# Kernel optimization log

Measured on AMD Instinct MI355X. Metric: run time of the kernel, lower is better.

Reference implementation:

```python
import jax, jax.numpy as jnp
import numpy as np

R_CUT = 5.0
N_NODES = 50000
N_EDGES = 400000
N_GRAPHS = 2500
D = 128        # embedding_size (hardcoded by torch.split(..., 128))
N_RBF = 20
N_BLOCKS = 3
PI = 3.141592653589793


def setup_inputs() -> dict:
    key = jax.random.key(0)
    ks = jax.random.split(key, 32)
    w = lambda k, s: (jax.random.normal(k, s) * 0.05).astype(jnp.float32)
    z = jax.random.randint(ks[0], (N_NODES,), 0, 100)
    edges = jax.random.randint(ks[1], (N_EDGES, 2), 0, N_NODES)
    r_ij = jax.random.uniform(ks[2], (N_EDGES, 1), minval=0.8, maxval=R_CUT, dtype=jnp.float32)
    d = jax.random.normal(ks[3], (N_EDGES, 3), dtype=jnp.float32)
    r_ij_normalized = d / jnp.linalg.norm(d, axis=1, keepdims=True)
    graph_idx = jax.random.randint(ks[4], (N_NODES,), 0, N_GRAPHS)
    return {
        "z": z, "edges": edges, "r_ij": r_ij,
        "r_ij_normalized": r_ij_normalized, "graph_idx": graph_idx,
        "emb": w(ks[5], (100, D)),
        # message blocks (stacked over N_BLOCKS)
        "msg_w1": w(ks[6], (N_BLOCKS, D, D)),   "msg_b1": w(ks[7], (N_BLOCKS, D)),
        "msg_w2": w(ks[8], (N_BLOCKS, D, 3 * D)), "msg_b2": w(ks[9], (N_BLOCKS, 3 * D)),
        "rbf_w": w(ks[10], (N_BLOCKS, N_RBF, 3 * D)), "rbf_b": w(ks[11], (N_BLOCKS, 3 * D)),
        # update blocks
        "upd_U": w(ks[12], (N_BLOCKS, D, D)), "upd_V": w(ks[13], (N_BLOCKS, D, D)),
        "upd_w1": w(ks[14], (N_BLOCKS, 2 * D, D)), "upd_b1": w(ks[15], (N_BLOCKS, D)),
        "upd_w2": w(ks[16], (N_BLOCKS, D, 3 * D)), "upd_b2": w(ks[17], (N_BLOCKS, 3 * D)),
        # readout
        "blue_w1": w(ks[18], (D, D)), "blue_b1": w(ks[19], (D,)),
        "blue_w2": w(ks[20], (D, 1)), "blue_b2": w(ks[21], (1,)),
    }


def _rbf(r, r_cut):
    n = jnp.arange(1, N_RBF + 1, dtype=r.dtype)  # [20]
    return jnp.sin(n * PI / r_cut * r) / r        # [E,20]


def _fcut(r, r_cut):
    return jnp.where(r <= r_cut, 0.5 * (jnp.cos(PI * r / r_cut) + 1.0), 0.0)


def painn_forward(z, edges, r_ij, r_ij_normalized, graph_idx, emb,
                  msg_w1, msg_b1, msg_w2, msg_b2, rbf_w, rbf_b,
                  upd_U, upd_V, upd_w1, upd_b1, upd_w2, upd_b2,
                  blue_w1, blue_b1, blue_w2, blue_b2):
    silu = jax.nn.silu
    src = edges[:, 1]  # gathered (neighbor j)
    dst = edges[:, 0]  # scattered (center i)
    s = emb[z]                                           # [N,128]
    v = jnp.zeros((s.shape[0], 3, D), dtype=r_ij.dtype)  # [N,3,128]
    rbf = _rbf(r_ij, R_CUT)                              # [E,20]
    f_c = _fcut(r_ij, R_CUT)                             # [E,1]
    for i in range(N_BLOCKS):
        # --- message block ---
        rbf_fcut = (rbf @ rbf_w[i] + rbf_b[i]) * f_c            # [E,384]
        s_pass = silu(s @ msg_w1[i] + msg_b1[i]) @ msg_w2[i] + msg_b2[i]  # [N,384]
        pass_out = rbf_fcut * s_pass[src]                        # [E,384]
        d_v, d_s, d_rep = jnp.split(pass_out, 3, axis=-1)        # each [E,128]
        delta_v = v[src] * d_v[:, None, :] + r_ij_normalized[:, :, None] * d_rep[:, None, :]
        s = s + jax.ops.segment_sum(d_s, dst, num_segments=N_NODES)
        v = v + jax.ops.segment_sum(delta_v, dst, num_segments=N_NODES)
        # --- update block ---
        U_v = jnp.einsum('nde,ef->ndf', v, upd_U[i])             # [N,3,128]
        V_v = jnp.einsum('nde,ef->ndf', v, upd_V[i])
        V_norm = jnp.linalg.norm(V_v, axis=1)                    # [N,128]
        sv = jnp.concatenate([V_norm, s], axis=1)                # [N,256]
        a = silu(sv @ upd_w1[i] + upd_b1[i]) @ upd_w2[i] + upd_b2[i]  # [N,384]
        avv, asv, ass = jnp.split(a, 3, axis=1)
        s = s + jnp.sum(U_v * V_v, axis=1) * asv + ass
        v = v + avv[:, None, :] * U_v
    blue = silu(s @ blue_w1 + blue_b1) @ blue_w2 + blue_b2       # [N,1]
    return jax.ops.segment_sum(blue, graph_idx, num_segments=N_GRAPHS)  # [G,1]


def reference(z, edges, r_ij, r_ij_normalized, graph_idx, emb,
              msg_w1, msg_b1, msg_w2, msg_b2, rbf_w, rbf_b,
              upd_U, upd_V, upd_w1, upd_b1, upd_w2, upd_b2,
              blue_w1, blue_b1, blue_w2, blue_b2):
    return painn_forward(z, edges, r_ij, r_ij_normalized, graph_idx, emb,
                         msg_w1, msg_b1, msg_w2, msg_b2, rbf_w, rbf_b,
                         upd_U, upd_V, upd_w1, upd_b1, upd_w2, upd_b2,
                         blue_w1, blue_b1, blue_w2, blue_b2)
```

## Files before the change

kernel.cpp:

```cpp
#include <hip/hip_runtime.h>
#include <hip/hip_bf16.h>
#include <math.h>

#define N_NODES 50000
#define N_EDGES 400000
#define N_GRAPHS 2500
#define D 128
#define D3 384
#define N_RBF 20
#define R_CUT 5.0f
#define PI_F 3.14159265358979f
#define NCH 98

typedef __attribute__((ext_vector_type(8))) short bf16x8;
typedef __attribute__((ext_vector_type(4))) float f32x4;

__device__ __forceinline__ float silu_f(float x) {
    return x / (1.0f + __expf(-x));
}
__device__ __forceinline__ short f2bf(float x) {
    union { float f; unsigned u; } v; v.f = x;
    unsigned r = (v.u + 0x7FFFu + ((v.u >> 16) & 1u)) >> 16;
    return (short)r;
}
__device__ __forceinline__ float bf2f(short x) {
    union { unsigned u; float f; } v; v.u = ((unsigned)(unsigned short)x) << 16;
    return v.f;
}

__global__ void k_pack(const float* __restrict__ W, short* __restrict__ P, int K, int N) {
    int t = blockIdx.x * 256 + threadIdx.x;
    int NKT = K / 32;
    int total = (N / 16) * NKT * 64;
    if (t >= total) return;
    int lane = t & 63;
    int kt = (t >> 6) % NKT;
    int nt = (t >> 6) / NKT;
    int k0 = kt * 32 + (lane >> 4) * 8;
    int col = nt * 16 + (lane & 15);
    #pragma unroll
    for (int j = 0; j < 8; ++j)
        P[(size_t)t * 8 + j] = f2bf(W[(size_t)(k0 + j) * N + col]);
}

template<int K, int N, bool SILU, int AMODE>
__global__ __launch_bounds__(256) void k_gemm(const void* __restrict__ Aptr,
                                              const void* __restrict__ A2ptr,
                                              const short* __restrict__ Bp,
                                              const float* __restrict__ bias,
                                              short* __restrict__ Cbf, int M) {
    constexpr int NKT = K / 32, NNT = N / 16;
    int lane = threadIdx.x & 63, wv = threadIdx.x >> 6;
    int tile = blockIdx.x * 4 + wv;
    if (tile * 16 >= M) return;
    int arow = tile * 16 + (lane & 15);
    int kgrp = (lane >> 4) * 8;

    bf16x8 a[NKT];
    if (AMODE == 0) {
        const short* A = (const short*)Aptr + (size_t)arow * K + kgrp;
        #pragma unroll
        for (int kt = 0; kt < NKT; ++kt) a[kt] = *(const bf16x8*)(A + kt * 32);
    } else if (AMODE == 1) {
        const float* A = (const float*)Aptr + (size_t)arow * K + kgrp;
        #pragma unroll
        for (int kt = 0; kt < NKT; ++kt)
            #pragma unroll
            for (int j = 0; j < 8; ++j) a[kt][j] = f2bf(A[kt * 32 + j]);
    } else {
        const short* A1 = (const short*)Aptr + (size_t)arow * 128 + kgrp;
        const float* A2 = (const float*)A2ptr + (size_t)arow * 128 + kgrp;
        #pragma unroll
        for (int kt = 0; kt < 4 && kt < NKT; ++kt) a[kt] = *(const bf16x8*)(A1 + kt * 32);
        #pragma unroll
        for (int kt = 4; kt < NKT; ++kt)
            #pragma unroll
            for (int j = 0; j < 8; ++j) a[kt][j] = f2bf(A2[(kt - 4) * 32 + j]);
    }

    int crow0 = tile * 16 + (lane >> 4) * 4;
    int ccol = lane & 15;
    const bf16x8* Bv = (const bf16x8*)Bp;
    #pragma unroll
    for (int nt = 0; nt < NNT; ++nt) {
        f32x4 acc = {0.f, 0.f, 0.f, 0.f};
        #pragma unroll
        for (int kt = 0; kt < NKT; ++kt) {
            bf16x8 b = Bv[(nt * NKT + kt) * 64 + lane];
            acc = __builtin_amdgcn_mfma_f32_16x16x32_bf16(a[kt], b, acc, 0, 0, 0);
        }
        int col = nt * 16 + ccol;
        float bs = bias ? bias[col] : 0.0f;
        #pragma unroll
        for (int j = 0; j < 4; ++j) {
            float v = acc[j] + bs;
            if (SILU) v = silu_f(v);
            Cbf[(size_t)(crow0 + j) * N + col] = f2bf(v);
        }
    }
}

__global__ void k_embed(const int* __restrict__ z, const float* __restrict__ emb,
                        float* __restrict__ s) {
    int i = blockIdx.x * blockDim.x + threadIdx.x;
    if (i < N_NODES * D) {
        int n = i >> 7, c = i & 127;
        s[i] = emb[z[n] * D + c];
    }
}

__global__ void k_hist(const int* __restrict__ edges, int* __restrict__ cnt) {
    int e = blockIdx.x * 256 + threadIdx.x;
    if (e < N_EDGES) atomicAdd(&cnt[edges[2 * e]], 1);
}

__global__ void k_scan1(const int* __restrict__ cnt, int* __restrict__ csum) {
    int t = threadIdx.x;
    int g = blockIdx.x * 512 + t;
    int v = (g < N_NODES) ? cnt[g] : 0;
    #pragma unroll
    for (int off = 32; off > 0; off >>= 1) v += __shfl_down(v, off, 64);
    __shared__ int ws[8];
    if ((t & 63) == 0) ws[t >> 6] = v;
    __syncthreads();
    if (t == 0) {
        int sum = 0;
        #pragma unroll
        for (int i = 0; i < 8; ++i) sum += ws[i];
        csum[blockIdx.x] = sum;
    }
}

__global__ void k_scan2(const int* __restrict__ csum, int* __restrict__ cbase) {
    if (threadIdx.x == 0 && blockIdx.x == 0) {
        int s = 0;
        for (int i = 0; i < NCH; ++i) { cbase[i] = s; s += csum[i]; }
    }
}

__global__ void k_scan3(const int* __restrict__ cnt, const int* __restrict__ cbase,
                        int* __restrict__ rowptr) {
    __shared__ int buf[512];
    int t = threadIdx.x;
    int g = blockIdx.x * 512 + t;
    int orig = (g < N_NODES) ? cnt[g] : 0;
    buf[t] = orig;
    __syncthreads();
    for (int off = 1; off < 512; off <<= 1) {
        int v = (t >= off) ? buf[t - off] : 0;
        __syncthreads();
        buf[t] += v;
        __syncthreads();
    }
    if (g < N_NODES) rowptr[g] = cbase[blockIdx.x] + buf[t] - orig;
    if (g == 0 && blockIdx.x == 0) rowptr[N_NODES] = N_EDGES;
}

__global__ void k_scatter(const int* __restrict__ edges, const float* __restrict__ r_ij,
                          const float* __restrict__ rhat, const int* __restrict__ rowptr,
                          int* __restrict__ cursor, int* __restrict__ esrc,
                          float4* __restrict__ efr, short* __restrict__ erbf) {
    int e = blockIdx.x * 256 + threadIdx.x;
    if (e >= N_EDGES) return;
    int dst = edges[2 * e], src = edges[2 * e + 1];
    int p = rowptr[dst] + atomicAdd(&cursor[dst], 1);
    esrc[p] = src;
    float r = r_ij[e];
    float fc = (r <= R_CUT) ? 0.5f * (cosf(PI_F * r / R_CUT) + 1.0f) : 0.0f;
    float4 fr;
    fr.x = fc; fr.y = rhat[3 * e]; fr.z = rhat[3 * e + 1]; fr.w = rhat[3 * e + 2];
    efr[p] = fr;
    float inv_r = 1.0f / r;
    #pragma unroll
    for (int k = 0; k < N_RBF; ++k) {
        float rb = sinf((float)(k + 1) * (PI_F / R_CUT) * r) * inv_r;
        erbf[(size_t)p * 24 + k] = f2bf(rb * fc);
    }
}

__global__ __launch_bounds__(128) void k_edge2(
    const int* __restrict__ rowptr, const int* __restrict__ esrc,
    const float4* __restrict__ efr, const short* __restrict__ erbf,
    const float* __restrict__ rbf_w, const float* __restrict__ rbf_b,
    const short* __restrict__ spass, const short* __restrict__ vold,
    float* __restrict__ s, short* __restrict__ vnew) {
    int c = threadIdx.x;
    float w0[N_RBF], w1[N_RBF], w2[N_RBF];
    #pragma unroll
    for (int k = 0; k < N_RBF; ++k) {
        w0[k] = rbf_w[k * D3 + c];
        w1[k] = rbf_w[k * D3 + 128 + c];
        w2[k] = rbf_w[k * D3 + 256 + c];
    }
    float b0 = rbf_b[c], b1 = rbf_b[128 + c], b2 = rbf_b[256 + c];
    for (int n = blockIdx.x; n < N_NODES; n += gridDim.x) {
        int p0 = rowptr[n], p1 = rowptr[n + 1];
        float sa = 0.f, va0 = 0.f, va1 = 0.f, va2 = 0.f;
        for (int p = p0; p < p1; ++p) {
            bf16x8 rA = *(const bf16x8*)(erbf + (size_t)p * 24);
            bf16x8 rB = *(const bf16x8*)(erbf + (size_t)p * 24 + 8);
            bf16x8 rC = *(const bf16x8*)(erbf + (size_t)p * 24 + 16);
            float4 fr = efr[p];
            int src = esrc[p];
            float a0 = 0.f, a1 = 0.f, a2 = 0.f;
            #pragma unroll
            for (int k = 0; k < 8; ++k) {
                float rv = bf2f(rA[k]);
                a0 += rv * w0[k]; a1 += rv * w1[k]; a2 += rv * w2[k];
            }
            #pragma unroll
            for (int k = 0; k < 8; ++k) {
                float rv = bf2f(rB[k]);
                a0 += rv * w0[8 + k]; a1 += rv * w1[8 + k]; a2 += rv * w2[8 + k];
            }
            #pragma unroll
            for (int k = 0; k < 4; ++k) {
                float rv = bf2f(rC[k]);
                a0 += rv * w0[16 + k]; a1 += rv * w1[16 + k]; a2 += rv * w2[16 + k];
            }
            a0 += b0 * fr.x; a1 += b1 * fr.x; a2 += b2 * fr.x;
            const short* sp = spass + (size_t)src * D3;
            float dv = a0 * bf2f(sp[c]);
            float ds = a1 * bf2f(sp[128 + c]);
            float dr = a2 * bf2f(sp[256 + c]);
            sa += ds;
            const short* vs = vold + (size_t)src * D3;
            va0 += bf2f(vs[c]) * dv + fr.y * dr;
            va1 += bf2f(vs[128 + c]) * dv + fr.z * dr;
            va2 += bf2f(vs[256 + c]) * dv + fr.w * dr;
        }
        s[(size_t)n * D + c] += sa;
        size_t vb = (size_t)n * D3;
        vnew[vb + c]       = f2bf(bf2f(vold[vb + c]) + va0);
        vnew[vb + 128 + c] = f2bf(bf2f(vold[vb + 128 + c]) + va1);
        vnew[vb + 256 + c] = f2bf(bf2f(vold[vb + 256 + c]) + va2);
    }
}

__global__ void k_svbuild(const short* __restrict__ Vv, short* __restrict__ Vn) {
    int i = blockIdx.x * 256 + threadIdx.x;
    int n = i >> 7, c = i & 127;
    float acc = 0.f;
    #pragma unroll
    for (int d = 0; d < 3; ++d) {
        float v = bf2f(Vv[(size_t)(n * 3 + d) * D + c]);
        acc += v * v;
    }
    Vn[i] = f2bf(sqrtf(acc));
}

__global__ void k_apply(float* __restrict__ s, short* __restrict__ v,
                        const short* __restrict__ Uv, const short* __restrict__ Vv,
                        const short* __restrict__ a_bf) {
    int i = blockIdx.x * 256 + threadIdx.x;
    int n = i >> 7, c = i & 127;
    float avv = bf2f(a_bf[(size_t)n * D3 + c]);
    float asv = bf2f(a_bf[(size_t)n * D3 + 128 + c]);
    float ass = bf2f(a_bf[(size_t)n * D3 + 256 + c]);
    float scal = 0.f;
    float uvr[3];
    #pragma unroll
    for (int d = 0; d < 3; ++d) {
        float u = bf2f(Uv[(size_t)(n * 3 + d) * D + c]);
        float vv = bf2f(Vv[(size_t)(n * 3 + d) * D + c]);
        uvr[d] = u;
        scal += u * vv;
    }
    s[i] += scal * asv + ass;
    #pragma unroll
    for (int d = 0; d < 3; ++d) {
        size_t idx = (size_t)n * D3 + d * 128 + c;
        v[idx] = f2bf(bf2f(v[idx]) + avv * uvr[d]);
    }
}

__global__ void k_blue_dot(const short* __restrict__ h, const int* __restrict__ graph_idx,
                           const float* __restrict__ w2, const float* __restrict__ b2,
                           float* __restrict__ out) {
    __shared__ float red[4];
    int c = threadIdx.x & 127;
    int n = blockIdx.x * 2 + (threadIdx.x >> 7);
    float val = bf2f(h[(size_t)n * D + c]) * w2[c];
    #pragma unroll
    for (int off = 32; off > 0; off >>= 1) val += __shfl_down(val, off, 64);
    if ((threadIdx.x & 63) == 0) red[threadIdx.x >> 6] = val;
    __syncthreads();
    if (threadIdx.x == 0)   atomicAdd(&out[graph_idx[n]], red[0] + red[1] + b2[0]);
    if (threadIdx.x == 128) atomicAdd(&out[graph_idx[n]], red[2] + red[3] + b2[0]);
}

static inline int gemm_grid(int M) { return (M / 16 + 3) / 4; }

extern "C" void kernel_launch(void* const* d_in, const int* in_sizes, int n_in,
                              void* d_out, int out_size, void* d_ws, size_t ws_size,
                              hipStream_t stream) {
    const int*   z         = (const int*)d_in[0];
    const int*   edges     = (const int*)d_in[1];
    const float* r_ij      = (const float*)d_in[2];
    const float* rhat      = (const float*)d_in[3];
    const int*   graph_idx = (const int*)d_in[4];
    const float* emb       = (const float*)d_in[5];
    const float* msg_w1    = (const float*)d_in[6];
    const float* msg_b1    = (const float*)d_in[7];
    const float* msg_w2    = (const float*)d_in[8];
    const float* msg_b2    = (const float*)d_in[9];
    const float* rbf_w     = (const float*)d_in[10];
    const float* rbf_b     = (const float*)d_in[11];
    const float* upd_U     = (const float*)d_in[12];
    const float* upd_V     = (const float*)d_in[13];
    const float* upd_w1    = (const float*)d_in[14];
    const float* upd_b1    = (const float*)d_in[15];
    const float* upd_w2    = (const float*)d_in[16];
    const float* upd_b2    = (const float*)d_in[17];
    const float* blue_w1   = (const float*)d_in[18];
    const float* blue_b1   = (const float*)d_in[19];
    const float* blue_w2   = (const float*)d_in[20];
    const float* blue_b2   = (const float*)d_in[21];
    float* out = (float*)d_out;

    char* ws = (char*)d_ws;
    size_t off = 0;
    auto alloc = [&](size_t bytes) { void* p = ws + off; off += (bytes + 255) & ~(size_t)255; return p; };

    float* s      = (float*)alloc((size_t)N_NODES * D * 4);
    short* bufV0  = (short*)alloc((size_t)N_NODES * D3 * 2);
    short* bufV1  = (short*)alloc((size_t)N_NODES * D3 * 2);
    short* shrd   = (short*)alloc((size_t)N_NODES * D3 * 2);
    short* hbuf   = (short*)alloc((size_t)N_NODES * D * 2);
    short* Vn     = (short*)alloc((size_t)N_NODES * D * 2);
    short* Vv     = (short*)alloc((size_t)N_NODES * D3 * 2);
    int*    esrc   = (int*)alloc((size_t)N_EDGES * 4);
    float4* efr    = (float4*)alloc((size_t)N_EDGES * 16);
    short*  erbf   = (short*)alloc((size_t)N_EDGES * 24 * 2);
    int*    rowptr = (int*)alloc((size_t)(N_NODES + 1) * 4);
    int*    cnt    = (int*)alloc((size_t)N_NODES * 4);
    int*    csum   = (int*)alloc(NCH * 4);
    int*    cbase  = (int*)alloc(NCH * 4);

    short* pBlue = (short*)alloc(16384 * 2);
    short* pMsgW1[3]; short* pMsgW2[3]; short* pU[3]; short* pV[3]; short* pUpdW1[3]; short* pUpdW2[3];
    for (int i = 0; i < 3; ++i) {
        pMsgW1[i] = (short*)alloc(16384 * 2);
        pMsgW2[i] = (short*)alloc(49152 * 2);
        pU[i]     = (short*)alloc(16384 * 2);
        pV[i]     = (short*)alloc(16384 * 2);
        pUpdW1[i] = (short*)alloc(32768 * 2);
        pUpdW2[i] = (short*)alloc(49152 * 2);
    }

    auto pack = [&](const float* W, short* P, int K, int N) {
        int total = (N / 16) * (K / 32) * 64;
        k_pack<<<(total + 255) / 256, 256, 0, stream>>>(W, P, K, N);
    };
    pack(blue_w1, pBlue, 128, 128);
    for (int i = 0; i < 3; ++i) {
        pack(msg_w1 + (size_t)i * D * D,     pMsgW1[i], 128, 128);
        pack(msg_w2 + (size_t)i * D * D3,    pMsgW2[i], 128, 384);
        pack(upd_U  + (size_t)i * D * D,     pU[i],     128, 128);
        pack(upd_V  + (size_t)i * D * D,     pV[i],     128, 128);
        pack(upd_w1 + (size_t)i * 2 * D * D, pUpdW1[i], 256, 128);
        pack(upd_w2 + (size_t)i * D * D3,    pUpdW2[i], 128, 384);
    }

    hipMemsetAsync(cnt, 0, (size_t)N_NODES * 4, stream);
    k_hist<<<(N_EDGES + 255) / 256, 256, 0, stream>>>(edges, cnt);
    k_scan1<<<NCH, 512, 0, stream>>>(cnt, csum);
    k_scan2<<<1, 64, 0, stream>>>(csum, cbase);
    k_scan3<<<NCH, 512, 0, stream>>>(cnt, cbase, rowptr);
    hipMemsetAsync(cnt, 0, (size_t)N_NODES * 4, stream);
    k_scatter<<<(N_EDGES + 255) / 256, 256, 0, stream>>>(edges, r_ij, rhat, rowptr, cnt,
                                                         esrc, efr, erbf);

    hipMemsetAsync(bufV0, 0, (size_t)N_NODES * D3 * 2, stream);
    hipMemsetAsync(d_out, 0, (size_t)out_size * sizeof(float), stream);
    k_embed<<<(N_NODES * D) / 256, 256, 0, stream>>>(z, emb, s);

    const int gN  = gemm_grid(N_NODES);
    const int gN3 = gemm_grid(N_NODES * 3);

    for (int i = 0; i < 3; ++i) {
        short* vstate = (i & 1) ? bufV1 : bufV0;
        short* vscr   = (i & 1) ? bufV0 : bufV1;
        k_gemm<128, 128, true, 1><<<gN, 256, 0, stream>>>(
            s, nullptr, pMsgW1[i], msg_b1 + (size_t)i * D, hbuf, N_NODES);
        k_gemm<128, 384, false, 0><<<gN, 256, 0, stream>>>(
            hbuf, nullptr, pMsgW2[i], msg_b2 + (size_t)i * D3, shrd, N_NODES);
        k_edge2<<<4096, 128, 0, stream>>>(rowptr, esrc, efr, erbf,
                                          rbf_w + (size_t)i * N_RBF * D3,
                                          rbf_b + (size_t)i * D3,
                                          shrd, vstate, s, vscr);
        k_gemm<128, 128, false, 0><<<gN3, 256, 0, stream>>>(
            vscr, nullptr, pU[i], nullptr, vstate, N_NODES * 3);
        k_gemm<128, 128, false, 0><<<gN3, 256, 0, stream>>>(
            vscr, nullptr, pV[i], nullptr, Vv, N_NODES * 3);
        k_svbuild<<<(N_NODES * D) / 256, 256, 0, stream>>>(Vv, Vn);
        k_gemm<256, 128, true, 2><<<gN, 256, 0, stream>>>(
            Vn, s, pUpdW1[i], upd_b1 + (size_t)i * D, hbuf, N_NODES);
        k_gemm<128, 384, false, 0><<<gN, 256, 0, stream>>>(
            hbuf, nullptr, pUpdW2[i], upd_b2 + (size_t)i * D3, shrd, N_NODES);
        k_apply<<<(N_NODES * D) / 256, 256, 0, stream>>>(s, vscr, vstate, Vv, shrd);
    }

    k_gemm<128, 128, true, 1><<<gN, 256, 0, stream>>>(
        s, nullptr, pBlue, blue_b1, hbuf, N_NODES);
    k_blue_dot<<<N_NODES / 2, 256, 0, stream>>>(hbuf, graph_idx, blue_w2, blue_b2, out);
}
```

Before: 1.195 ms.

## Batch weight packing into one launch and store edge RBF records as fp32

Replaces the 19 separate weight-pack kernel launches with a single job-table kernel, which cuts launch overhead. Merges the bf16 RBF array and the float4 edge-feature array into one 24-float fp32 record per edge, so the edge kernel reads six float4 loads with no bf16 conversion. Adds a launch-bounds occupancy hint to the edge kernel and aliases the Vn buffer onto shrd to shrink the workspace. The fp32 record roughly doubles edge-feature bytes per edge read, and the Vn/shrd alias relies on shrd being dead while Vn is in use.

Result: no change. 1.174 ms (-1.8%).

```diff
diff --git a/kernel.cpp b/kernel.cpp
--- a/kernel.cpp
+++ b/kernel.cpp
@@ -11,6 +11,7 @@
 #define R_CUT 5.0f
 #define PI_F 3.14159265358979f
 #define NCH 98
+#define EPT_STRIDE 24
 
 typedef __attribute__((ext_vector_type(8))) short bf16x8;
 typedef __attribute__((ext_vector_type(4))) float f32x4;
@@ -28,19 +29,34 @@
     return v.f;
 }
 
-__global__ void k_pack(const float* __restrict__ W, short* __restrict__ P, int K, int N) {
-    int t = blockIdx.x * 256 + threadIdx.x;
+#define MAXJOBS 19
+struct PackJobs {
+    const float* W[MAXJOBS];
+    short* P[MAXJOBS];
+    int K[MAXJOBS];
+    int N[MAXJOBS];
+    int boff[MAXJOBS + 1];
+    int njobs;
+};
+__global__ void k_packall(PackJobs jobs) {
+    int b = blockIdx.x;
+    int j = 0;
+    while (j + 1 < jobs.njobs && b >= jobs.boff[j + 1]) ++j;
+    int t = (b - jobs.boff[j]) * 256 + threadIdx.x;
+    int K = jobs.K[j], N = jobs.N[j];
     int NKT = K / 32;
     int total = (N / 16) * NKT * 64;
     if (t >= total) return;
+    const float* W = jobs.W[j];
+    short* P = jobs.P[j];
     int lane = t & 63;
     int kt = (t >> 6) % NKT;
     int nt = (t >> 6) / NKT;
     int k0 = kt * 32 + (lane >> 4) * 8;
     int col = nt * 16 + (lane & 15);
     #pragma unroll
-    for (int j = 0; j < 8; ++j)
-        P[(size_t)t * 8 + j] = f2bf(W[(size_t)(k0 + j) * N + col]);
+    for (int q = 0; q < 8; ++q)
+        P[(size_t)t * 8 + q] = f2bf(W[(size_t)(k0 + q) * N + col]);
 }
 
 template<int K, int N, bool SILU, int AMODE>
@@ -159,7 +175,7 @@
 __global__ void k_scatter(const int* __restrict__ edges, const float* __restrict__ r_ij,
                           const float* __restrict__ rhat, const int* __restrict__ rowptr,
                           int* __restrict__ cursor, int* __restrict__ esrc,
-                          float4* __restrict__ efr, short* __restrict__ erbf) {
+                          float* __restrict__ ept) {
     int e = blockIdx.x * 256 + threadIdx.x;
     if (e >= N_EDGES) return;
     int dst = edges[2 * e], src = edges[2 * e + 1];
@@ -167,20 +183,22 @@
     esrc[p] = src;
     float r = r_ij[e];
     float fc = (r <= R_CUT) ? 0.5f * (cosf(PI_F * r / R_CUT) + 1.0f) : 0.0f;
-    float4 fr;
-    fr.x = fc; fr.y = rhat[3 * e]; fr.z = rhat[3 * e + 1]; fr.w = rhat[3 * e + 2];
-    efr[p] = fr;
     float inv_r = 1.0f / r;
+    float* rec = ept + (size_t)p * EPT_STRIDE;
     #pragma unroll
     for (int k = 0; k < N_RBF; ++k) {
         float rb = sinf((float)(k + 1) * (PI_F / R_CUT) * r) * inv_r;
-        erbf[(size_t)p * 24 + k] = f2bf(rb * fc);
-    }
-}
-
-__global__ __launch_bounds__(128) void k_edge2(
+        rec[k] = rb * fc;
+    }
+    rec[20] = fc;
+    rec[21] = rhat[3 * e];
+    rec[22] = rhat[3 * e + 1];
+    rec[23] = rhat[3 * e + 2];
+}
+
+__global__ __launch_bounds__(128, 4) void k_edge2(
     const int* __restrict__ rowptr, const int* __restrict__ esrc,
-    const float4* __restrict__ efr, const short* __restrict__ erbf,
+    const float* __restrict__ ept,
     const float* __restrict__ rbf_w, const float* __restrict__ rbf_b,
     const short* __restrict__ spass, const short* __restrict__ vold,
     float* __restrict__ s, short* __restrict__ vnew) {
@@ -197,37 +215,30 @@
         int p0 = rowptr[n], p1 = rowptr[n + 1];
         float sa = 0.f, va0 = 0.f, va1 = 0.f, va2 = 0.f;
         for (int p = p0; p < p1; ++p) {
-            bf16x8 rA = *(const bf16x8*)(erbf + (size_t)p * 24);
-            bf16x8 rB = *(const bf16x8*)(erbf + (size_t)p * 24 + 8);
-            bf16x8 rC = *(const bf16x8*)(erbf + (size_t)p * 24 + 16);
-            float4 fr = efr[p];
+            const float4* e4 = (const float4*)(ept + (size_t)p * EPT_STRIDE);
+            float4 q0 = e4[0], q1 = e4[1], q2 = e4[2], q3 = e4[3], q4 = e4[4], q5 = e4[5];
             int src = esrc[p];
-            float a0 = 0.f, a1 = 0.f, a2 = 0.f;
+            float a0, a1, a2;
+            float fc = q5.x;
+            a0 = b0 * fc; a1 = b1 * fc; a2 = b2 * fc;
+            float rv[20] = {q0.x, q0.y, q0.z, q0.w, q1.x, q1.y, q1.z, q1.w,
+                            q2.x, q2.y, q2.z, q2.w, q3.x, q3.y, q3.z, q3.w,
+                            q4.x, q4.y, q4.z, q4.w};
             #pragma unroll
-            for (int k = 0; k < 8; ++k) {
-                float rv = bf2f(rA[k]);
-                a0 += rv * w0[k]; a1 += rv * w1[k]; a2 += rv * w2[k];
+            for (int k = 0; k < N_RBF; ++k) {
+                a0 += rv[k] * w0[k];
+                a1 += rv[k] * w1[k];
+                a2 += rv[k] * w2[k];
             }
-            #pragma unroll
-            for (int k = 0; k < 8; ++k) {
-                float rv = bf2f(rB[k]);
-                a0 += rv * w0[8 + k]; a1 += rv * w1[8 + k]; a2 += rv * w2[8 + k];
-            }
-            #pragma unroll
-            for (int k = 0; k < 4; ++k) {
-                float rv = bf2f(rC[k]);
-                a0 += rv * w0[16 + k]; a1 += rv * w1[16 + k]; a2 += rv * w2[16 + k];
-            }
-            a0 += b0 * fr.x; a1 += b1 * fr.x; a2 += b2 * fr.x;
             const short* sp = spass + (size_t)src * D3;
             float dv = a0 * bf2f(sp[c]);
             float ds = a1 * bf2f(sp[128 + c]);
             float dr = a2 * bf2f(sp[256 + c]);
             sa += ds;
             const short* vs = vold + (size_t)src * D3;
-            va0 += bf2f(vs[c]) * dv + fr.y * dr;
-            va1 += bf2f(vs[128 + c]) * dv + fr.z * dr;
-            va2 += bf2f(vs[256 + c]) * dv + fr.w * dr;
+            va0 += bf2f(vs[c]) * dv + q5.y * dr;
+            va1 += bf2f(vs[128 + c]) * dv + q5.z * dr;
+            va2 += bf2f(vs[256 + c]) * dv + q5.w * dr;
         }
         s[(size_t)n * D + c] += sa;
         size_t vb = (size_t)n * D3;
@@ -327,11 +338,10 @@
     short* bufV1  = (short*)alloc((size_t)N_NODES * D3 * 2);
     short* shrd   = (short*)alloc((size_t)N_NODES * D3 * 2);
     short* hbuf   = (short*)alloc((size_t)N_NODES * D * 2);
-    short* Vn     = (short*)alloc((size_t)N_NODES * D * 2);
     short* Vv     = (short*)alloc((size_t)N_NODES * D3 * 2);
+    short* Vn     = shrd;
     int*    esrc   = (int*)alloc((size_t)N_EDGES * 4);
-    float4* efr    = (float4*)alloc((size_t)N_EDGES * 16);
-    short*  erbf   = (short*)alloc((size_t)N_EDGES * 24 * 2);
+    float*  ept    = (float*)alloc((size_t)N_EDGES * EPT_STRIDE * 4);
     int*    rowptr = (int*)alloc((size_t)(N_NODES + 1) * 4);
     int*    cnt    = (int*)alloc((size_t)N_NODES * 4);
     int*    csum   = (int*)alloc(NCH * 4);
@@ -348,19 +358,27 @@
         pUpdW2[i] = (short*)alloc(49152 * 2);
     }
 
-    auto pack = [&](const float* W, short* P, int K, int N) {
+    PackJobs jobs;
+    jobs.njobs = 0;
+    int bacc = 0;
+    auto addjob = [&](const float* W, short* P, int K, int N) {
+        int j = jobs.njobs++;
+        jobs.W[j] = W; jobs.P[j] = P; jobs.K[j] = K; jobs.N[j] = N;
+        jobs.boff[j] = bacc;
         int total = (N / 16) * (K / 32) * 64;
-        k_pack<<<(total + 255) / 256, 256, 0, stream>>>(W, P, K, N);
+        bacc += (total + 255) / 256;
+        jobs.boff[j + 1] = bacc;
     };
-    pack(blue_w1, pBlue, 128, 128);
+    addjob(blue_w1, pBlue, 128, 128);
     for (int i = 0; i < 3; ++i) {
-        pack(msg_w1 + (size_t)i * D * D,     pMsgW1[i], 128, 128);
-        pack(msg_w2 + (size_t)i * D * D3,    pMsgW2[i], 128, 384);
-        pack(upd_U  + (size_t)i * D * D,     pU[i],     128, 128);
-        pack(upd_V  + (size_t)i * D * D,     pV[i],     128, 128);
-        pack(upd_w1 + (size_t)i * 2 * D * D, pUpdW1[i], 256, 128);
-        pack(upd_w2 + (size_t)i * D * D3,    pUpdW2[i], 128, 384);
-    }
+        addjob(msg_w1 + (size_t)i * D * D,     pMsgW1[i], 128, 128);
+        addjob(msg_w2 + (size_t)i * D * D3,    pMsgW2[i], 128, 384);
+        addjob(upd_U  + (size_t)i * D * D,     pU[i],     128, 128);
+        addjob(upd_V  + (size_t)i * D * D,     pV[i],     128, 128);
+        addjob(upd_w1 + (size_t)i * 2 * D * D, pUpdW1[i], 256, 128);
+        addjob(upd_w2 + (size_t)i * D * D3,    pUpdW2[i], 128, 384);
+    }
+    k_packall<<<bacc, 256, 0, stream>>>(jobs);
 
     hipMemsetAsync(cnt, 0, (size_t)N_NODES * 4, stream);
     k_hist<<<(N_EDGES + 255) / 256, 256, 0, stream>>>(edges, cnt);
@@ -369,7 +387,7 @@
     k_scan3<<<NCH, 512, 0, stream>>>(cnt, cbase, rowptr);
     hipMemsetAsync(cnt, 0, (size_t)N_NODES * 4, stream);
     k_scatter<<<(N_EDGES + 255) / 256, 256, 0, stream>>>(edges, r_ij, rhat, rowptr, cnt,
-                                                         esrc, efr, erbf);
+                                                         esrc, ept);
 
     hipMemsetAsync(bufV0, 0, (size_t)N_NODES * D3 * 2, stream);
     hipMemsetAsync(d_out, 0, (size_t)out_size * sizeof(float), stream);
@@ -385,7 +403,7 @@
             s, nullptr, pMsgW1[i], msg_b1 + (size_t)i * D, hbuf, N_NODES);
         k_gemm<128, 384, false, 0><<<gN, 256, 0, stream>>>(
             hbuf, nullptr, pMsgW2[i], msg_b2 + (size_t)i * D3, shrd, N_NODES);
-        k_edge2<<<4096, 128, 0, stream>>>(rowptr, esrc, efr, erbf,
+        k_edge2<<<4096, 128, 0, stream>>>(rowptr, esrc, ept,
                                           rbf_w + (size_t)i * N_RBF * D3,
                                           rbf_b + (size_t)i * D3,
                                           shrd, vstate, s, vscr);
```
